# Kernel tuning notes

Measured on AMD Instinct MI355X. Metric: run time of the kernel, lower is better.

## Reference

```python
import jax, jax.numpy as jnp
import numpy as np

SCALE = 16.0
TEMP = 0.07
EPS = 1e-8


def setup_inputs() -> dict:
    key = jax.random.key(0)
    k0, k1, k2, k3, k4 = jax.random.split(key, 5)
    B, D, h, w = 16, 128, 48, 48
    feats_a = jax.random.normal(k0, (B, D, h, w), jnp.float32)
    feats_b = jax.random.normal(k1, (B, D, h, w), jnp.float32)
    eye = jnp.eye(3, dtype=jnp.float32)
    # near-identity homographies (must be invertible)
    Hs_a = eye[None] + 0.02 * jax.random.normal(k2, (B, 3, 3), jnp.float32)
    Hs_b = eye[None] + 0.02 * jax.random.normal(k3, (B, 3, 3), jnp.float32)
    # near-identity affine with a small translation (in large-image pixels)
    M_a_b = jnp.array([[1.0, 0.0, 24.0], [0.0, 1.0, -16.0]], jnp.float32) \
        + 0.01 * jax.random.normal(k4, (2, 3), jnp.float32)
    return {"feats_a": feats_a, "feats_b": feats_b, "Hs_a": Hs_a, "Hs_b": Hs_b, "M_a_b": M_a_b}


def _transform_matrix(Hs_a, Hs_b, M_a_b):
    # Feat_A -> Img_A -> Large_A -> Large_B -> Img_B -> Feat_B
    B = Hs_a.shape[0]
    dt = Hs_a.dtype
    M3 = jnp.concatenate([M_a_b, jnp.array([[0.0, 0.0, 1.0]], dt)], axis=0)  # (3,3)
    S = jnp.diag(jnp.array([SCALE, SCALE, 1.0], dt))
    S_inv = jnp.diag(jnp.array([1.0 / SCALE, 1.0 / SCALE, 1.0], dt))
    Ha_inv = jnp.linalg.inv(Hs_a)  # (B,3,3)
    T = S_inv[None] @ Hs_b @ M3[None] @ Ha_inv @ S[None]
    return T


def _bilinear_sample(feats, grid):
    # feats (B,D,H,W); grid (B,h,w,2) normalized to [-1,1], align_corners=True,
    # zero padding for out-of-range samples (matches F.grid_sample).
    B, D, H, W = feats.shape
    h, w = grid.shape[1], grid.shape[2]
    ix = (grid[..., 0] + 1.0) * 0.5 * (W - 1)  # (B,h,w)
    iy = (grid[..., 1] + 1.0) * 0.5 * (H - 1)
    x0 = jnp.floor(ix); y0 = jnp.floor(iy)
    wx1 = ix - x0; wx0 = 1.0 - wx1
    wy1 = iy - y0; wy0 = 1.0 - wy1
    feats_flat = feats.reshape(B, D, H * W)

    def gather(xi, yi):
        valid = (xi >= 0) & (xi <= W - 1) & (yi >= 0) & (yi <= H - 1)
        xc = jnp.clip(xi, 0, W - 1).astype(jnp.int32)
        yc = jnp.clip(yi, 0, H - 1).astype(jnp.int32)
        idx = (yc * W + xc).reshape(B, -1)  # (B, h*w)
        v = jnp.take_along_axis(feats_flat, idx[:, None, :], axis=2)  # (B,D,h*w)
        return v * valid.reshape(B, 1, -1).astype(feats.dtype)

    out = (gather(x0, y0) * (wx0 * wy0).reshape(B, 1, -1)
           + gather(x0 + 1, y0) * (wx1 * wy0).reshape(B, 1, -1)
           + gather(x0, y0 + 1) * (wx0 * wy1).reshape(B, 1, -1)
           + gather(x0 + 1, y0 + 1) * (wx1 * wy1).reshape(B, 1, -1))
    return out.reshape(B, D, h, w)


def reference(feats_a, feats_b, Hs_a, Hs_b, M_a_b):
    B, D, h, w = feats_a.shape
    N = h * w
    H_b, W_b = feats_b.shape[2], feats_b.shape[3]
    T = _transform_matrix(Hs_a, Hs_b, M_a_b)  # (B,3,3)

    # homogeneous pixel grid of feats_a: (3, N)
    gy, gx = jnp.meshgrid(jnp.arange(h, dtype=jnp.float32), jnp.arange(w, dtype=jnp.float32), indexing='ij')
    coords = jnp.stack([gx.ravel(), gy.ravel(), jnp.ones(N, jnp.float32)], axis=0)  # (3,N)
    new = jnp.einsum('bij,jn->bin', T, coords)  # (B,3,N)
    z = new[:, 2, :] + EPS
    x_norm = 2.0 * (new[:, 0, :] / z) / (W_b - 1) - 1.0  # (B,N)
    y_norm = 2.0 * (new[:, 1, :] / z) / (H_b - 1) - 1.0
    grid = jnp.stack([x_norm, y_norm], axis=-1).reshape(B, h, w, 2)
    valid_mask = ((grid[..., 0] >= -1) & (grid[..., 0] <= 1)
                  & (grid[..., 1] >= -1) & (grid[..., 1] <= 1)).astype(jnp.float32)  # (B,h,w)

    warped_b = _bilinear_sample(feats_b, grid)  # (B,D,h,w)

    fa = feats_a.reshape(B, D, N).transpose(0, 2, 1)   # (B,N,D)
    wb = warped_b.reshape(B, D, N).transpose(0, 2, 1)  # (B,N,D)
    # F.normalize: x / max(||x||, eps) with eps=1e-12
    fa = fa / jnp.maximum(jnp.linalg.norm(fa, axis=2, keepdims=True), 1e-12)
    wb = wb / jnp.maximum(jnp.linalg.norm(wb, axis=2, keepdims=True), 1e-12)

    logits = jnp.einsum('bnd,bmd->bnm', fa, wb) / TEMP  # (B,N,N)
    # cross-entropy with labels = diagonal
    lse = jax.nn.logsumexp(logits, axis=-1)  # (B,N)
    diag = jnp.einsum('bnn->bn', logits)     # (B,N)
    loss_per = lse - diag                    # (B,N)

    mask = valid_mask.reshape(B, N)
    num_valid = mask.sum()
    total = (loss_per * mask).sum()
    return jnp.where(num_valid > 0, total / jnp.maximum(num_valid, 1.0), 0.0)
```

## Files before the change

kernel.cpp:

```cpp
#include <hip/hip_runtime.h>
#include <math.h>

#define B_ 16
#define D_ 128
#define HH 48
#define WW 48
#define N_ 2304
#define NC 72
#define SCALE_ 16.0f
#define INV_TEMP 14.285714285714286f
#define L2E_TEMP 20.60992915555662f
#define EPS_ 1e-8f
#define SPLITC 6
#define STAGES 6

typedef __attribute__((ext_vector_type(8))) short bf16x8;
typedef __attribute__((ext_vector_type(16))) float f32x16;

__device__ __forceinline__ short f2bf(float f) {
    union { float f; unsigned u; } v; v.f = f;
    unsigned r = v.u + 0x7FFFu + ((v.u >> 16) & 1u);
    return (short)(r >> 16);
}

__device__ __forceinline__ size_t frag_off(int b, int c, int ks, int lane) {
    return ((((size_t)b * NC + c) * 8 + ks) << 9) + (size_t)lane * 8;
}

__device__ __forceinline__ void gld16(const short* g, short* l) {
    __builtin_amdgcn_global_load_lds(
        (const __attribute__((address_space(1))) void*)g,
        (__attribute__((address_space(3))) void*)l, 16, 0, 0);
}

__global__ __launch_bounds__(256) void k_prep(const float* __restrict__ fa,
                                              const float* __restrict__ fb,
                                              const float* __restrict__ Ha,
                                              const float* __restrict__ Hb,
                                              const float* __restrict__ Mab,
                                              float* __restrict__ maskA,
                                              short* __restrict__ faF,
                                              short* __restrict__ wbF) {
    __shared__ float part[4][2][32];
    const int b = blockIdx.y;
    const int rb = blockIdx.x;
    const int n0 = rb * 32;
    const int tid = threadIdx.x;
    const int lane = tid & 63, wv = tid >> 6;
    const int r = lane & 31, h = lane >> 5;
    const int n = n0 + r;

    float T[9];
    {
        const float* A = Ha + b * 9;
        const float* Bm = Hb + b * 9;
        float c00 = A[4] * A[8] - A[5] * A[7];
        float c01 = A[5] * A[6] - A[3] * A[8];
        float c02 = A[3] * A[7] - A[4] * A[6];
        float id = 1.f / (A[0] * c00 + A[1] * c01 + A[2] * c02);
        float inv[9] = { c00 * id, (A[2] * A[7] - A[1] * A[8]) * id, (A[1] * A[5] - A[2] * A[4]) * id,
                         c01 * id, (A[0] * A[8] - A[2] * A[6]) * id, (A[2] * A[3] - A[0] * A[5]) * id,
                         c02 * id, (A[1] * A[6] - A[0] * A[7]) * id, (A[0] * A[4] - A[1] * A[3]) * id };
        float M3[9] = {Mab[0], Mab[1], Mab[2], Mab[3], Mab[4], Mab[5], 0.f, 0.f, 1.f};
        float P1[9], P2[9];
        for (int i = 0; i < 3; ++i)
            for (int j = 0; j < 3; ++j) {
                float s = 0.f;
                for (int k = 0; k < 3; ++k) s += Bm[i * 3 + k] * M3[k * 3 + j];
                P1[i * 3 + j] = s;
            }
        for (int i = 0; i < 3; ++i)
            for (int j = 0; j < 3; ++j) {
                float s = 0.f;
                for (int k = 0; k < 3; ++k) s += P1[i * 3 + k] * inv[k * 3 + j];
                P2[i * 3 + j] = s;
            }
        const float sc[3] = {SCALE_, SCALE_, 1.f};
        for (int i = 0; i < 3; ++i)
            for (int j = 0; j < 3; ++j) T[i * 3 + j] = P2[i * 3 + j] * sc[j] / sc[i];
    }

    const float gx = (float)(n % WW), gy = (float)(n / WW);
    const float X = T[0] * gx + T[1] * gy + T[2];
    const float Y = T[3] * gx + T[4] * gy + T[5];
    const float z = T[6] * gx + T[7] * gy + T[8] + EPS_;
    const float xn = 2.f * (X / z) / (float)(WW - 1) - 1.f;
    const float yn = 2.f * (Y / z) / (float)(HH - 1) - 1.f;
    const float msk = (xn >= -1.f && xn <= 1.f && yn >= -1.f && yn <= 1.f) ? 1.f : 0.f;
    const float ix = (xn + 1.f) * 0.5f * (float)(WW - 1);
    const float iy = (yn + 1.f) * 0.5f * (float)(HH - 1);
    const float x0f = floorf(ix), y0f = floorf(iy);
    const float wx1 = ix - x0f, wx0 = 1.f - wx1;
    const float wy1 = iy - y0f, wy0 = 1.f - wy1;
    const bool vx0 = (x0f >= 0.f) && (x0f <= 47.f);
    const bool vx1 = (x0f + 1.f >= 0.f) && (x0f + 1.f <= 47.f);
    const bool vy0 = (y0f >= 0.f) && (y0f <= 47.f);
    const bool vy1 = (y0f + 1.f >= 0.f) && (y0f + 1.f <= 47.f);
    const float w00 = (vx0 && vy0) ? wx0 * wy0 : 0.f;
    const float w01 = (vx1 && vy0) ? wx1 * wy0 : 0.f;
    const float w10 = (vx0 && vy1) ? wx0 * wy1 : 0.f;
    const float w11 = (vx1 && vy1) ? wx1 * wy1 : 0.f;
    const int x0c = (int)fminf(fmaxf(x0f, 0.f), 47.f);
    const int x1c = (int)fminf(fmaxf(x0f + 1.f, 0.f), 47.f);
    const int y0c = (int)fminf(fmaxf(y0f, 0.f), 47.f);
    const int y1c = (int)fminf(fmaxf(y0f + 1.f, 0.f), 47.f);
    const int o00 = y0c * WW + x0c, o01 = y0c * WW + x1c;
    const int o10 = y1c * WW + x0c, o11 = y1c * WW + x1c;

    const float* fab = fa + (size_t)b * D_ * N_;
    const float* fbb = fb + (size_t)b * D_ * N_;

    float av[2][8], wvv[2][8];
    float sA = 0.f, sW = 0.f;
    #pragma unroll
    for (int g = 0; g < 2; ++g) {
        const int ks = wv + 4 * g;
        const int dbase = ks * 16 + h * 8;
        #pragma unroll
        for (int j = 0; j < 8; ++j) {
            const int d = dbase + j;
            const float* p = fbb + (size_t)d * N_;
            float w = w00 * p[o00] + w01 * p[o01] + w10 * p[o10] + w11 * p[o11];
            float a = fab[(size_t)d * N_ + n];
            av[g][j] = a; wvv[g][j] = w;
            sA += a * a; sW += w * w;
        }
    }
    sA += __shfl_xor(sA, 32);
    sW += __shfl_xor(sW, 32);
    if (lane < 32) { part[wv][0][r] = sA; part[wv][1][r] = sW; }
    if (tid < 32) maskA[b * N_ + n0 + r] = msk;
    __syncthreads();
    const float rnA = 1.f / fmaxf(sqrtf(part[0][0][r] + part[1][0][r] + part[2][0][r] + part[3][0][r]), 1e-12f);
    const float rnW = 1.f / fmaxf(sqrtf(part[0][1][r] + part[1][1][r] + part[2][1][r] + part[3][1][r]), 1e-12f);

    #pragma unroll
    for (int g = 0; g < 2; ++g) {
        const int ks = wv + 4 * g;
        bf16x8 oa, ow;
        #pragma unroll
        for (int j = 0; j < 8; ++j) {
            oa[j] = f2bf(av[g][j] * rnA);
            ow[j] = f2bf(wvv[g][j] * rnW);
        }
        size_t off = frag_off(b, rb, ks, lane);
        *(bf16x8*)(faF + off) = oa;
        *(bf16x8*)(wbF + off) = ow;
    }
}

__global__ __launch_bounds__(256, 2) void k_loss(const short* __restrict__ faF,
                                                 const short* __restrict__ wbF,
                                                 float* __restrict__ Zpart,
                                                 float* __restrict__ dgbuf) {
    __shared__ short bbuf[2][8192];
    __shared__ float s_Z[256];
    const int lin = blockIdx.x;
    const int xcd = lin & 7;
    const int i0 = lin >> 3;
    const int b = xcd * 2 + (i0 / 54);
    const int r54 = i0 % 54;
    const int bx = r54 % 9;
    const int cs = r54 / 9;
    const int tid = threadIdx.x;
    const int lane = tid & 63, w = tid >> 6;
    const int l31 = lane & 31, h = lane >> 5;
    const int rc0 = bx * 8 + w * 2;
    const int rc1 = rc0 + 1;

    bf16x8 af0[8], af1[8];
    #pragma unroll
    for (int ks = 0; ks < 8; ++ks) {
        af0[ks] = *(const bf16x8*)(faF + frag_off(b, rc0, ks, lane));
        af1[ks] = *(const bf16x8*)(faF + frag_off(b, rc1, ks, lane));
    }

    float Z0[16], Z1[16];
    #pragma unroll
    for (int i = 0; i < 16; ++i) { Z0[i] = 0.f; Z1[i] = 0.f; }

    const short* bsrc = wbF + frag_off(b, cs * 12, 0, 0);

    #define STAGE_B(nb, s) { \
        const short* sg = bsrc + (size_t)(s) * 8192 + w * 2048 + lane * 8; \
        short* sl = &bbuf[nb][w * 2048]; \
        _Pragma("unroll") \
        for (int j = 0; j < 4; ++j) gld16(sg + j * 512, sl + j * 512); \
    }

    STAGE_B(0, 0);
    __syncthreads();

    for (int s = 0; s < STAGES; ++s) {
        if (s + 1 < STAGES) STAGE_B((s + 1) & 1, s + 1);
        const short* bb = &bbuf[s & 1][0];
        f32x16 C00, C01, C10, C11;
        #pragma unroll
        for (int i = 0; i < 16; ++i) { C00[i] = 0.f; C01[i] = 0.f; C10[i] = 0.f; C11[i] = 0.f; }
        #pragma unroll
        for (int ks = 0; ks < 8; ++ks) {
            bf16x8 b0 = *(const bf16x8*)(bb + ks * 512 + lane * 8);
            bf16x8 b1 = *(const bf16x8*)(bb + 4096 + ks * 512 + lane * 8);
            C00 = __builtin_amdgcn_mfma_f32_32x32x16_bf16(af0[ks], b0, C00, 0, 0, 0);
            C10 = __builtin_amdgcn_mfma_f32_32x32x16_bf16(af1[ks], b0, C10, 0, 0, 0);
            C01 = __builtin_amdgcn_mfma_f32_32x32x16_bf16(af0[ks], b1, C01, 0, 0, 0);
            C11 = __builtin_amdgcn_mfma_f32_32x32x16_bf16(af1[ks], b1, C11, 0, 0, 0);
        }
        #pragma unroll
        for (int i = 0; i < 16; ++i) {
            Z0[i] += exp2f(fmaf(C00[i], L2E_TEMP, -L2E_TEMP))
                   + exp2f(fmaf(C01[i], L2E_TEMP, -L2E_TEMP));
            Z1[i] += exp2f(fmaf(C10[i], L2E_TEMP, -L2E_TEMP))
                   + exp2f(fmaf(C11[i], L2E_TEMP, -L2E_TEMP));
        }
        const int jc0 = cs * 12 + 2 * s, jc1 = jc0 + 1;
        if (jc0 == rc0) {
            #pragma unroll
            for (int i = 0; i < 16; ++i) {
                int rr = (i & 3) + 8 * (i >> 2) + 4 * h;
                if (l31 == rr) dgbuf[b * N_ + rc0 * 32 + rr] = INV_TEMP * C00[i];
            }
        }
        if (jc1 == rc1) {
            #pragma unroll
            for (int i = 0; i < 16; ++i) {
                int rr = (i & 3) + 8 * (i >> 2) + 4 * h;
                if (l31 == rr) dgbuf[b * N_ + rc1 * 32 + rr] = INV_TEMP * C11[i];
            }
        }
        __syncthreads();
    }
    #undef STAGE_B

    #pragma unroll
    for (int i = 0; i < 16; ++i) {
        float z0 = Z0[i], z1 = Z1[i];
        #pragma unroll
        for (int off = 1; off < 32; off <<= 1) {
            z0 += __shfl_xor(z0, off);
            z1 += __shfl_xor(z1, off);
        }
        if (l31 == 0) {
            int rr = (i & 3) + 8 * (i >> 2) + 4 * h;
            s_Z[w * 64 + rr] = z0;
            s_Z[w * 64 + 32 + rr] = z1;
        }
    }
    __syncthreads();
    Zpart[((size_t)cs * B_ + b) * N_ + bx * 256 + tid] = s_Z[tid];
}

__global__ __launch_bounds__(256) void k_pass2(const float* __restrict__ maskA,
                                               const float* __restrict__ Zpart,
                                               const float* __restrict__ dgbuf,
                                               float* __restrict__ partials) {
    const int idx = blockIdx.x * 256 + threadIdx.x;
    float Zs = 0.f;
    #pragma unroll
    for (int s = 0; s < SPLITC; ++s) Zs += Zpart[(size_t)s * B_ * N_ + idx];
    const float m = maskA[idx];
    float lossv = (logf(Zs) + INV_TEMP - dgbuf[idx]) * m;
    float cm = m;
    for (int off = 1; off < 64; off <<= 1) {
        lossv += __shfl_xor(lossv, off);
        cm += __shfl_xor(cm, off);
    }
    __shared__ float s[8];
    const int wv = threadIdx.x >> 6;
    if ((threadIdx.x & 63) == 0) { s[wv * 2] = lossv; s[wv * 2 + 1] = cm; }
    __syncthreads();
    if (threadIdx.x == 0) {
        partials[blockIdx.x * 2] = s[0] + s[2] + s[4] + s[6];
        partials[blockIdx.x * 2 + 1] = s[1] + s[3] + s[5] + s[7];
    }
}

__global__ void k_final(const float* __restrict__ partials, float* __restrict__ out) {
    const int t = threadIdx.x;
    float tt = 0.f, cc = 0.f;
    for (int i = t; i < 144; i += 64) { tt += partials[i * 2]; cc += partials[i * 2 + 1]; }
    for (int off = 1; off < 64; off <<= 1) {
        tt += __shfl_xor(tt, off);
        cc += __shfl_xor(cc, off);
    }
    if (t == 0) out[0] = (cc > 0.f) ? tt / fmaxf(cc, 1.f) : 0.f;
}

extern "C" void kernel_launch(void* const* d_in, const int* in_sizes, int n_in,
                              void* d_out, int out_size, void* d_ws, size_t ws_size,
                              hipStream_t stream) {
    const float* fa = (const float*)d_in[0];
    const float* fb = (const float*)d_in[1];
    const float* Ha = (const float*)d_in[2];
    const float* Hb = (const float*)d_in[3];
    const float* M = (const float*)d_in[4];
    float* out = (float*)d_out;

    float* wsf = (float*)d_ws;
    float* Zpart = wsf;
    float* dgbuf = Zpart + (size_t)SPLITC * B_ * N_;
    float* maskA = dgbuf + B_ * N_;
    float* partials = maskA + B_ * N_;
    short* faF = (short*)(partials + 512);
    short* wbF = faF + (size_t)B_ * NC * 8 * 512;

    hipLaunchKernelGGL(k_prep, dim3(NC, B_), dim3(256), 0, stream,
                       fa, fb, Ha, Hb, M, maskA, faF, wbF);
    hipLaunchKernelGGL(k_loss, dim3(8 * 108), dim3(256), 0, stream,
                       faF, wbF, Zpart, dgbuf);
    hipLaunchKernelGGL(k_pass2, dim3(B_ * N_ / 256), dim3(256), 0, stream,
                       maskA, Zpart, dgbuf, partials);
    hipLaunchKernelGGL(k_final, dim3(1), dim3(64), 0, stream, partials, out);
}
```

Baseline: 149.1 us.

## Double column split, cut accumulator registers, raise occupancy in loss kernel

```diff
diff --git a/kernel.cpp b/kernel.cpp
--- a/kernel.cpp
+++ b/kernel.cpp
@@ -11,8 +11,8 @@
 #define INV_TEMP 14.285714285714286f
 #define L2E_TEMP 20.60992915555662f
 #define EPS_ 1e-8f
-#define SPLITC 6
-#define STAGES 6
+#define SPLITC 12
+#define STAGES 3
 
 typedef __attribute__((ext_vector_type(8))) short bf16x8;
 typedef __attribute__((ext_vector_type(16))) float f32x16;
@@ -149,7 +149,7 @@
     }
 }
 
-__global__ __launch_bounds__(256, 2) void k_loss(const short* __restrict__ faF,
+__global__ __launch_bounds__(256, 3) void k_loss(const short* __restrict__ faF,
                                                  const short* __restrict__ wbF,
                                                  float* __restrict__ Zpart,
                                                  float* __restrict__ dgbuf) {
@@ -158,10 +158,10 @@
     const int lin = blockIdx.x;
     const int xcd = lin & 7;
     const int i0 = lin >> 3;
-    const int b = xcd * 2 + (i0 / 54);
-    const int r54 = i0 % 54;
-    const int bx = r54 % 9;
-    const int cs = r54 / 9;
+    const int b = xcd * 2 + (i0 / 108);
+    const int r108 = i0 % 108;
+    const int bx = r108 % 9;
+    const int cs = r108 / 9;
     const int tid = threadIdx.x;
     const int lane = tid & 63, w = tid >> 6;
     const int l31 = lane & 31, h = lane >> 5;
@@ -179,7 +179,7 @@
     #pragma unroll
     for (int i = 0; i < 16; ++i) { Z0[i] = 0.f; Z1[i] = 0.f; }
 
-    const short* bsrc = wbF + frag_off(b, cs * 12, 0, 0);
+    const short* bsrc = wbF + frag_off(b, cs * 6, 0, 0);
 
     #define STAGE_B(nb, s) { \
         const short* sg = bsrc + (size_t)(s) * 8192 + w * 2048 + lane * 8; \
@@ -191,41 +191,42 @@
     STAGE_B(0, 0);
     __syncthreads();
 
+    #pragma unroll
     for (int s = 0; s < STAGES; ++s) {
         if (s + 1 < STAGES) STAGE_B((s + 1) & 1, s + 1);
         const short* bb = &bbuf[s & 1][0];
-        f32x16 C00, C01, C10, C11;
         #pragma unroll
-        for (int i = 0; i < 16; ++i) { C00[i] = 0.f; C01[i] = 0.f; C10[i] = 0.f; C11[i] = 0.f; }
-        #pragma unroll
-        for (int ks = 0; ks < 8; ++ks) {
-            bf16x8 b0 = *(const bf16x8*)(bb + ks * 512 + lane * 8);
-            bf16x8 b1 = *(const bf16x8*)(bb + 4096 + ks * 512 + lane * 8);
-            C00 = __builtin_amdgcn_mfma_f32_32x32x16_bf16(af0[ks], b0, C00, 0, 0, 0);
-            C10 = __builtin_amdgcn_mfma_f32_32x32x16_bf16(af1[ks], b0, C10, 0, 0, 0);
-            C01 = __builtin_amdgcn_mfma_f32_32x32x16_bf16(af0[ks], b1, C01, 0, 0, 0);
-            C11 = __builtin_amdgcn_mfma_f32_32x32x16_bf16(af1[ks], b1, C11, 0, 0, 0);
-        }
-        #pragma unroll
-        for (int i = 0; i < 16; ++i) {
-            Z0[i] += exp2f(fmaf(C00[i], L2E_TEMP, -L2E_TEMP))
-                   + exp2f(fmaf(C01[i], L2E_TEMP, -L2E_TEMP));
-            Z1[i] += exp2f(fmaf(C10[i], L2E_TEMP, -L2E_TEMP))
-                   + exp2f(fmaf(C11[i], L2E_TEMP, -L2E_TEMP));
-        }
-        const int jc0 = cs * 12 + 2 * s, jc1 = jc0 + 1;
-        if (jc0 == rc0) {
+        for (int c = 0; c < 2; ++c) {
+            const int jc = cs * 6 + 2 * s + c;
+            f32x16 C0, C1;
+            #pragma unroll
+            for (int i = 0; i < 16; ++i) { C0[i] = 0.f; C1[i] = 0.f; }
+            __builtin_amdgcn_s_setprio(1);
+            #pragma unroll
+            for (int ks = 0; ks < 8; ++ks) {
+                bf16x8 bf = *(const bf16x8*)(bb + c * 4096 + ks * 512 + lane * 8);
+                C0 = __builtin_amdgcn_mfma_f32_32x32x16_bf16(af0[ks], bf, C0, 0, 0, 0);
+                C1 = __builtin_amdgcn_mfma_f32_32x32x16_bf16(af1[ks], bf, C1, 0, 0, 0);
+            }
+            __builtin_amdgcn_s_setprio(0);
             #pragma unroll
             for (int i = 0; i < 16; ++i) {
-                int rr = (i & 3) + 8 * (i >> 2) + 4 * h;
-                if (l31 == rr) dgbuf[b * N_ + rc0 * 32 + rr] = INV_TEMP * C00[i];
-            }
-        }
-        if (jc1 == rc1) {
-            #pragma unroll
-            for (int i = 0; i < 16; ++i) {
-                int rr = (i & 3) + 8 * (i >> 2) + 4 * h;
-                if (l31 == rr) dgbuf[b * N_ + rc1 * 32 + rr] = INV_TEMP * C11[i];
+                Z0[i] += exp2f(fmaf(C0[i], L2E_TEMP, -L2E_TEMP));
+                Z1[i] += exp2f(fmaf(C1[i], L2E_TEMP, -L2E_TEMP));
+            }
+            if (jc == rc0) {
+                #pragma unroll
+                for (int i = 0; i < 16; ++i) {
+                    int rr = (i & 3) + 8 * (i >> 2) + 4 * h;
+                    if (l31 == rr) dgbuf[b * N_ + rc0 * 32 + rr] = INV_TEMP * C0[i];
+                }
+            }
+            if (jc == rc1) {
+                #pragma unroll
+                for (int i = 0; i < 16; ++i) {
+                    int rr = (i & 3) + 8 * (i >> 2) + 4 * h;
+                    if (l31 == rr) dgbuf[b * N_ + rc1 * 32 + rr] = INV_TEMP * C1[i];
+                }
             }
         }
         __syncthreads();
@@ -306,7 +307,7 @@
 
     hipLaunchKernelGGL(k_prep, dim3(NC, B_), dim3(256), 0, stream,
                        fa, fb, Ha, Hb, M, maskA, faF, wbF);
-    hipLaunchKernelGGL(k_loss, dim3(8 * 108), dim3(256), 0, stream,
+    hipLaunchKernelGGL(k_loss, dim3(8 * 216), dim3(256), 0, stream,
                        faF, wbF, Zpart, dgbuf);
     hipLaunchKernelGGL(k_pass2, dim3(B_ * N_ / 256), dim3(256), 0, stream,
                        maskA, Zpart, dgbuf, partials);
```

Measured after the change: 286.9 us. 92.5% more time.
